# Optimization experiments

Measured on AMD Instinct MI355X. Metric: run time of the kernel, lower is better.

The kernel has to match this reference:

```python
import jax, jax.numpy as jnp
import numpy as np

B, Q, C = 1024, 300, 80   # batch, queries, classes
K = 300                   # num_top_queries


def setup_inputs() -> dict:
    key = jax.random.key(0)
    k1, k2, k3 = jax.random.split(key, 3)
    pred_logits = jax.random.normal(k1, (B, Q, C), dtype=jnp.float32)
    # cxcywh boxes normalized to [0,1]
    pred_boxes = jax.random.uniform(k2, (B, Q, 4), dtype=jnp.float32)
    # original image sizes (w, h) in pixels
    orig_target_sizes = jax.random.uniform(k3, (B, 2), dtype=jnp.float32) * 1333.0 + 1.0
    return {"pred_logits": pred_logits, "pred_boxes": pred_boxes,
            "orig_target_sizes": orig_target_sizes}


def reference(pred_logits, pred_boxes, orig_target_sizes):
    # box_convert cxcywh -> xyxy
    cx, cy, w, h = jnp.split(pred_boxes, 4, axis=-1)
    xyxy = jnp.concatenate([cx - 0.5 * w, cy - 0.5 * h,
                            cx + 0.5 * w, cy + 0.5 * h], axis=-1)  # [B,Q,4]
    # scale by (w,h,w,h) per image
    scale = jnp.tile(orig_target_sizes, (1, 2))[:, None, :]          # [B,1,4]
    bbox_pred = xyxy * scale                                         # [B,Q,4]

    # focal-loss branch: sigmoid + flattened topk
    scores_flat = jax.nn.sigmoid(pred_logits).reshape(B, Q * C)      # [B,Q*C]
    top_scores, index = jax.lax.top_k(scores_flat, K)                # [B,K]
    labels = index % C                                               # class id
    qidx = index // C                                                # query id
    boxes = jnp.take_along_axis(bbox_pred, qidx[..., None], axis=1)  # [B,K,4]
    return labels, boxes, top_scores
```

## Files before the change

kernel.cpp:

```cpp
#include <hip/hip_runtime.h>
#include <stdint.h>

#define NBATCH 1024
#define NQ 300
#define NC 80
#define QC 24000
#define NF4 6000
#define TOPK 300
#define RSEL 384u
#define NT 256
#define LG (NT / 64)
#define NV 24
#define TAIL 112
#define NB1 2048
#define SH1 21
#define SH2 13
#define SELCAP 2048
#define FINCAP 768
#define THRESH 2.0f
#define NBH 2048
#define RG (NBH / NT)
#define SBASE 0x3F600000u

__device__ __forceinline__ uint32_t xform(uint32_t u) {
    return u ^ (uint32_t)(((int32_t)u >> 31) | 0x80000000);
}

__device__ __forceinline__ uint32_t sbucket(uint32_t sbits) {
    int32_t d = (int32_t)(sbits - SBASE);
    d = d < 0 ? 0 : d;
    uint32_t bkt = ((uint32_t)d) >> 10;
    return bkt > (NBH - 1) ? (NBH - 1) : bkt;
}

template<int NB, bool ZERO>
__device__ __forceinline__ void pick(uint32_t* __restrict__ hist,
                                     uint32_t* __restrict__ part,
                                     uint32_t* __restrict__ gsufx,
                                     uint32_t* __restrict__ misc,
                                     int tid, uint32_t rem,
                                     uint32_t* bucket_out, uint32_t* rem_out) {
    constexpr int G = (NB >= NT) ? (NB / NT) : 1;
    const int base = tid * G;
    uint32_t h[G];
    uint32_t s = 0;
    if (base < NB) {
#pragma unroll
        for (int u = 0; u < G; ++u) { h[u] = hist[base + u]; s += h[u]; }
        if (ZERO) {
#pragma unroll
            for (int u = 0; u < G; ++u) hist[base + u] = 0;
        }
    } else {
#pragma unroll
        for (int u = 0; u < G; ++u) h[u] = 0;
    }
    part[tid] = s;
    __syncthreads();

    if (tid < 64) {
        uint32_t gs = 0;
#pragma unroll
        for (int u = 0; u < LG; ++u) gs += part[tid * LG + u];
        uint32_t S = gs;
#pragma unroll
        for (int off = 1; off < 64; off <<= 1) {
            uint32_t v = __shfl_down(S, off, 64);
            if (tid + off < 64) S += v;
        }
        gsufx[tid] = S;
        if (tid == 0) gsufx[64] = 0;
    }
    __syncthreads();

    const int g = tid / LG;
    uint32_t A = gsufx[g + 1];
    for (int t2 = tid + 1; t2 < (g + 1) * LG; ++t2) A += part[t2];
    if (base < NB && A < rem && A + s >= rem) {
        uint32_t acc = 0, bsel = (uint32_t)base, r = 1;
#pragma unroll
        for (int u = G - 1; u >= 0; --u) {
            if (A + acc + h[u] >= rem) { bsel = (uint32_t)(base + u); r = rem - A - acc; break; }
            acc += h[u];
        }
        misc[0] = bsel;
        misc[1] = r;
    }
    __syncthreads();
    *bucket_out = misc[0];
    *rem_out    = misc[1];
}

__global__ void __launch_bounds__(NT, 4)
rtdetr_post_kernel(const float* __restrict__ logits, const float* __restrict__ pboxes,
                   const float* __restrict__ sizes, float* __restrict__ out) {
    __shared__ __align__(16) uint32_t hist[NBH + 1];
    __shared__ uint64_t sel[SELCAP];
    __shared__ uint64_t sel2[FINCAP];
    __shared__ uint32_t part[NT];
    __shared__ uint32_t gsufx[65];
    __shared__ uint32_t misc[4];

    const int tid = threadIdx.x;
    const int b   = blockIdx.x;
    const float4* lg4 = reinterpret_cast<const float4*>(logits + (size_t)b * QC);

    for (int i = tid; i <= NBH; i += NT) hist[i] = 0;
    if (tid == 0) { misc[2] = 0; misc[3] = 0; }
    __syncthreads();

#pragma unroll
    for (int k = 0; k < NV; ++k) {
        if (k < NV - 1 || tid < TAIL) {
            const int i4 = tid + (k << 8);
            float4 v = lg4[i4];
            float f[4] = { v.x, v.y, v.z, v.w };
#pragma unroll
            for (int c = 0; c < 4; ++c) {
                if (f[c] >= THRESH) {
                    uint32_t key = xform(__float_as_uint(f[c]));
                    uint32_t pos = atomicAdd(&misc[2], 1u);
                    uint32_t idx = 4u * (uint32_t)i4 + (uint32_t)c;
                    if (pos < SELCAP)
                        sel[pos] = ((uint64_t)key << 32) | (uint64_t)(0xFFFFFFFFu - idx);
                }
            }
        }
    }
    __syncthreads();

    const uint32_t cnt = misc[2];
    uint32_t n2;

    if (cnt >= RSEL && cnt <= FINCAP) {
        for (uint32_t i = tid; i < cnt; i += NT) {
            uint64_t e = sel[i];
            uint32_t k = (uint32_t)(e >> 32);
            uint32_t bits = (k & 0x80000000u) ? (k & 0x7FFFFFFFu) : ~k;
            float x  = __uint_as_float(bits);
            float sc = 1.0f / (1.0f + expf(-x));
            sel2[i] = ((uint64_t)__float_as_uint(sc) << 32) | (uint64_t)(uint32_t)e;
        }
        n2 = cnt;
    } else {
        if (tid == 0) misc[2] = 0;
        __syncthreads();
        for (int i4 = tid; i4 < NF4; i4 += NT) {
            float4 v = lg4[i4];
            atomicAdd(&hist[xform(__float_as_uint(v.x)) >> SH1], 1u);
            atomicAdd(&hist[xform(__float_as_uint(v.y)) >> SH1], 1u);
            atomicAdd(&hist[xform(__float_as_uint(v.z)) >> SH1], 1u);
            atomicAdd(&hist[xform(__float_as_uint(v.w)) >> SH1], 1u);
        }
        __syncthreads();
        uint32_t b1, r1;
        pick<NB1, true>(hist, part, gsufx, misc, tid, RSEL, &b1, &r1);
        for (int i4 = tid; i4 < NF4; i4 += NT) {
            float4 v = lg4[i4];
            uint32_t kk[4] = { xform(__float_as_uint(v.x)), xform(__float_as_uint(v.y)),
                               xform(__float_as_uint(v.z)), xform(__float_as_uint(v.w)) };
#pragma unroll
            for (int c = 0; c < 4; ++c) {
                uint32_t k = kk[c];
                uint32_t bk = k >> SH1;
                if (bk >= b1) {
                    uint32_t pos = atomicAdd(&misc[2], 1u);
                    uint32_t idx = 4u * (uint32_t)i4 + (uint32_t)c;
                    if (pos < SELCAP)
                        sel[pos] = ((uint64_t)k << 32) | (uint64_t)(0xFFFFFFFFu - idx);
                    if (bk == b1) atomicAdd(&hist[(k >> SH2) & 0xFFu], 1u);
                }
            }
        }
        __syncthreads();
        uint32_t t2, r2;
        pick<256, false>(hist, part, gsufx, misc, tid, r1, &t2, &r2);
        (void)r2;
        const uint32_t T2 = (b1 << SH1) | (t2 << SH2);
        uint32_t c2 = misc[2];
        uint32_t nn = c2 > SELCAP ? SELCAP : c2;
        for (uint32_t i = tid; i < nn; i += NT) {
            uint64_t e = sel[i];
            uint32_t k = (uint32_t)(e >> 32);
            if (k >= T2) {
                uint32_t bits = (k & 0x80000000u) ? (k & 0x7FFFFFFFu) : ~k;
                float x  = __uint_as_float(bits);
                float sc = 1.0f / (1.0f + expf(-x));
                uint32_t pos = atomicAdd(&misc[3], 1u);
                if (pos < FINCAP)
                    sel2[pos] = ((uint64_t)__float_as_uint(sc) << 32) | (uint64_t)(uint32_t)e;
            }
        }
        __syncthreads();
        uint32_t m3 = misc[3];
        n2 = m3 > FINCAP ? FINCAP : m3;
        for (int i = tid; i < 256; i += NT) hist[i] = 0;
    }
    __syncthreads();

    for (uint32_t i = tid; i < n2; i += NT)
        atomicAdd(&hist[sbucket((uint32_t)(sel2[i] >> 32))], 1u);
    __syncthreads();

    {
        const int base = tid * RG;
        uint32_t h[RG];
        uint32_t s = 0;
#pragma unroll
        for (int u = 0; u < RG; ++u) { h[u] = hist[base + u]; s += h[u]; }
        part[tid] = s;
        __syncthreads();
        if (tid < 64) {
            uint32_t gs = 0;
#pragma unroll
            for (int u = 0; u < LG; ++u) gs += part[tid * LG + u];
            uint32_t S = gs;
#pragma unroll
            for (int off = 1; off < 64; off <<= 1) {
                uint32_t v = __shfl_down(S, off, 64);
                if (tid + off < 64) S += v;
            }
            gsufx[tid] = S;
            if (tid == 0) gsufx[64] = 0;
        }
        __syncthreads();
        const int g = tid / LG;
        uint32_t A = gsufx[g + 1];
        for (int t2 = tid + 1; t2 < (g + 1) * LG; ++t2) A += part[t2];
        uint32_t acc = A;
#pragma unroll
        for (int u = RG - 1; u >= 0; --u) { hist[base + u] = acc; acc += h[u]; }
    }
    __syncthreads();

    for (uint32_t i = tid; i < n2; i += NT) {
        uint64_t k = sel2[i];
        uint32_t slot = atomicAdd(&hist[sbucket((uint32_t)(k >> 32))], 1u);
        sel[slot] = k;
    }
    __syncthreads();

    for (uint32_t i = tid; i < n2; i += NT) {
        uint64_t my = sel2[i];
        uint32_t bkt = sbucket((uint32_t)(my >> 32));
        uint32_t seg0 = hist[bkt + 1];
        uint32_t seg1 = hist[bkt];
        uint32_t rank = seg0;
        for (uint32_t j = seg0; j < seg1; ++j)
            rank += (sel[j] > my) ? 1u : 0u;
        if (rank < TOPK) {
            uint32_t idx = 0xFFFFFFFFu - (uint32_t)(my & 0xFFFFFFFFull);
            uint32_t lab = idx % NC;
            uint32_t q   = idx / NC;
            float4 bx = reinterpret_cast<const float4*>(pboxes)[(size_t)b * NQ + q];
            float sw = sizes[2 * b + 0];
            float sh = sizes[2 * b + 1];
            float hw = 0.5f * bx.z, hh = 0.5f * bx.w;
            float4 o;
            o.x = (bx.x - hw) * sw;
            o.y = (bx.y - hh) * sh;
            o.z = (bx.x + hw) * sw;
            o.w = (bx.y + hh) * sh;
            out[(size_t)b * TOPK + rank] = (float)lab;
            reinterpret_cast<float4*>(out + (size_t)NBATCH * TOPK)[(size_t)b * TOPK + rank] = o;
            out[(size_t)NBATCH * TOPK * 5 + (size_t)b * TOPK + rank] =
                __uint_as_float((uint32_t)(my >> 32));
        }
    }
}

extern "C" void kernel_launch(void* const* d_in, const int* in_sizes, int n_in,
                              void* d_out, int out_size, void* d_ws, size_t ws_size,
                              hipStream_t stream) {
    const float* logits = (const float*)d_in[0];
    const float* pboxes = (const float*)d_in[1];
    const float* sizes  = (const float*)d_in[2];
    float* out = (float*)d_out;

    hipLaunchKernelGGL(rtdetr_post_kernel, dim3(NBATCH), dim3(NT), 0, stream,
                       logits, pboxes, sizes, out);
}
```

Before: 28.75 us.

## Split logits threshold scan into a multi-block streaming kernel plus a per-batch select kernel

The single per-batch kernel is split in two. The first kernel gives each batch row's logits to four blocks, which threshold-filter candidates into a global workspace with per-slice counts. The second kernel gathers those candidates into shared memory and runs the radix-select and rank. It also handles candidate counts up to SELCAP on the in-LDS path by taking histograms over the candidates instead of re-reading the logits, with a full rescan kept as the fallback. The aim is to spread the bandwidth-bound scan across four times as many blocks, at the cost of an extra launch and a workspace round trip.

```diff
diff --git a/kernel.cpp b/kernel.cpp
--- a/kernel.cpp
+++ b/kernel.cpp
@@ -8,10 +8,14 @@
 #define NF4 6000
 #define TOPK 300
 #define RSEL 384u
+#define NSLICE 4
+#define SELEM 6000
+#define SF4 1500
+#define NT1 256
+#define SEGCAP 768
 #define NT 256
 #define LG (NT / 64)
-#define NV 24
-#define TAIL 112
+#define RG (2048 / NT)
 #define NB1 2048
 #define SH1 21
 #define SH2 13
@@ -19,7 +23,6 @@
 #define FINCAP 768
 #define THRESH 2.0f
 #define NBH 2048
-#define RG (NBH / NT)
 #define SBASE 0x3F600000u
 
 __device__ __forceinline__ uint32_t xform(uint32_t u) {
@@ -31,6 +34,46 @@
     d = d < 0 ? 0 : d;
     uint32_t bkt = ((uint32_t)d) >> 10;
     return bkt > (NBH - 1) ? (NBH - 1) : bkt;
+}
+
+__global__ void __launch_bounds__(NT1, 8)
+k1_stream(const float* __restrict__ logits, uint32_t* __restrict__ cnts,
+          uint64_t* __restrict__ buf) {
+    __shared__ uint32_t scnt;
+    __shared__ uint64_t sbuf[SEGCAP];
+    const int tid = threadIdx.x;
+    const int blk = blockIdx.x;
+    const int b   = blk >> 2;
+    const int sl  = blk & 3;
+    const float4* lg4 = reinterpret_cast<const float4*>(logits + (size_t)b * QC) + sl * SF4;
+
+    if (tid == 0) scnt = 0;
+    __syncthreads();
+
+#pragma unroll
+    for (int k = 0; k < 6; ++k) {
+        const int i4 = tid + (k << 8);
+        if (k < 5 || i4 < SF4) {
+            float4 v = lg4[i4];
+            float f[4] = { v.x, v.y, v.z, v.w };
+#pragma unroll
+            for (int c = 0; c < 4; ++c) {
+                if (f[c] >= THRESH) {
+                    uint32_t key = xform(__float_as_uint(f[c]));
+                    uint32_t idx = (uint32_t)(sl * SELEM) + 4u * (uint32_t)i4 + (uint32_t)c;
+                    uint32_t pos = atomicAdd(&scnt, 1u);
+                    if (pos < SEGCAP)
+                        sbuf[pos] = ((uint64_t)key << 32) | (uint64_t)(0xFFFFFFFFu - idx);
+                }
+            }
+        }
+    }
+    __syncthreads();
+    const uint32_t n = scnt;
+    if (tid == 0) cnts[blk] = n;
+    const uint32_t m = n > SEGCAP ? SEGCAP : n;
+    for (uint32_t i = tid; i < m; i += NT1)
+        buf[(size_t)blk * SEGCAP + i] = sbuf[i];
 }
 
 template<int NB, bool ZERO>
@@ -92,59 +135,100 @@
 }
 
 __global__ void __launch_bounds__(NT, 4)
-rtdetr_post_kernel(const float* __restrict__ logits, const float* __restrict__ pboxes,
-                   const float* __restrict__ sizes, float* __restrict__ out) {
+k2_select(const float* __restrict__ logits, const float* __restrict__ pboxes,
+          const float* __restrict__ sizes, const uint32_t* __restrict__ cnts,
+          const uint64_t* __restrict__ buf, float* __restrict__ out) {
     __shared__ __align__(16) uint32_t hist[NBH + 1];
-    __shared__ uint64_t sel[SELCAP];
-    __shared__ uint64_t sel2[FINCAP];
+    __shared__ uint64_t cand[SELCAP];
+    __shared__ uint64_t srt[FINCAP];
     __shared__ uint32_t part[NT];
     __shared__ uint32_t gsufx[65];
     __shared__ uint32_t misc[4];
+    __shared__ uint32_t soff[NSLICE];
+    __shared__ uint32_t sinfo[2];
 
     const int tid = threadIdx.x;
     const int b   = blockIdx.x;
     const float4* lg4 = reinterpret_cast<const float4*>(logits + (size_t)b * QC);
 
     for (int i = tid; i <= NBH; i += NT) hist[i] = 0;
-    if (tid == 0) { misc[2] = 0; misc[3] = 0; }
-    __syncthreads();
-
-#pragma unroll
-    for (int k = 0; k < NV; ++k) {
-        if (k < NV - 1 || tid < TAIL) {
-            const int i4 = tid + (k << 8);
-            float4 v = lg4[i4];
-            float f[4] = { v.x, v.y, v.z, v.w };
-#pragma unroll
-            for (int c = 0; c < 4; ++c) {
-                if (f[c] >= THRESH) {
-                    uint32_t key = xform(__float_as_uint(f[c]));
-                    uint32_t pos = atomicAdd(&misc[2], 1u);
-                    uint32_t idx = 4u * (uint32_t)i4 + (uint32_t)c;
-                    if (pos < SELCAP)
-                        sel[pos] = ((uint64_t)key << 32) | (uint64_t)(0xFFFFFFFFu - idx);
-                }
-            }
-        }
-    }
-    __syncthreads();
-
-    const uint32_t cnt = misc[2];
+    if (tid == 0) {
+        uint32_t tot = 0, trunc = 0;
+        for (int s = 0; s < NSLICE; ++s) {
+            uint32_t c = cnts[b * NSLICE + s];
+            soff[s] = tot;
+            tot += c;
+            if (c > SEGCAP) trunc = 1;
+        }
+        sinfo[0] = tot; sinfo[1] = trunc;
+        misc[2] = 0; misc[3] = 0;
+    }
+    __syncthreads();
+
+    const uint32_t cnt   = sinfo[0];
+    const uint32_t trunc = sinfo[1];
+    const bool ldsResident = (!trunc && cnt <= SELCAP && cnt >= RSEL);
+
+    if (!trunc && cnt <= SELCAP) {
+#pragma unroll
+        for (int s = 0; s < NSLICE; ++s) {
+            uint32_t c = cnts[b * NSLICE + s];
+            uint32_t o = soff[s];
+            const uint64_t* src = buf + (size_t)(b * NSLICE + s) * SEGCAP;
+            for (uint32_t i = tid; i < c; i += NT) cand[o + i] = src[i];
+        }
+    }
+    __syncthreads();
+
     uint32_t n2;
 
-    if (cnt >= RSEL && cnt <= FINCAP) {
+    if (ldsResident && cnt <= FINCAP) {
         for (uint32_t i = tid; i < cnt; i += NT) {
-            uint64_t e = sel[i];
+            uint64_t e = cand[i];
             uint32_t k = (uint32_t)(e >> 32);
             uint32_t bits = (k & 0x80000000u) ? (k & 0x7FFFFFFFu) : ~k;
             float x  = __uint_as_float(bits);
             float sc = 1.0f / (1.0f + expf(-x));
-            sel2[i] = ((uint64_t)__float_as_uint(sc) << 32) | (uint64_t)(uint32_t)e;
+            uint32_t sb = __float_as_uint(sc);
+            srt[i] = ((uint64_t)sb << 32) | (uint64_t)(uint32_t)e;
+            atomicAdd(&hist[sbucket(sb)], 1u);
         }
         n2 = cnt;
+    } else if (ldsResident) {
+        for (uint32_t i = tid; i < cnt; i += NT)
+            atomicAdd(&hist[(uint32_t)(cand[i] >> 32) >> SH1], 1u);
+        __syncthreads();
+        uint32_t b1, r1;
+        pick<NB1, true>(hist, part, gsufx, misc, tid, RSEL, &b1, &r1);
+        for (uint32_t i = tid; i < cnt; i += NT) {
+            uint32_t k = (uint32_t)(cand[i] >> 32);
+            if ((k >> SH1) == b1) atomicAdd(&hist[(k >> SH2) & 0xFFu], 1u);
+        }
+        __syncthreads();
+        uint32_t t2, r2;
+        pick<256, false>(hist, part, gsufx, misc, tid, r1, &t2, &r2);
+        (void)r2;
+        const uint32_t T2 = (b1 << SH1) | (t2 << SH2);
+        for (uint32_t i = tid; i < cnt; i += NT) {
+            uint64_t e = cand[i];
+            uint32_t k = (uint32_t)(e >> 32);
+            if (k >= T2) {
+                uint32_t bits = (k & 0x80000000u) ? (k & 0x7FFFFFFFu) : ~k;
+                float x  = __uint_as_float(bits);
+                float sc = 1.0f / (1.0f + expf(-x));
+                uint32_t pos = atomicAdd(&misc[3], 1u);
+                if (pos < FINCAP)
+                    srt[pos] = ((uint64_t)__float_as_uint(sc) << 32) | (uint64_t)(uint32_t)e;
+            }
+        }
+        __syncthreads();
+        uint32_t m3 = misc[3];
+        n2 = m3 > FINCAP ? FINCAP : m3;
+        for (int i = tid; i < 256; i += NT) hist[i] = 0;
+        __syncthreads();
+        for (uint32_t i = tid; i < n2; i += NT)
+            atomicAdd(&hist[sbucket((uint32_t)(srt[i] >> 32))], 1u);
     } else {
-        if (tid == 0) misc[2] = 0;
-        __syncthreads();
         for (int i4 = tid; i4 < NF4; i4 += NT) {
             float4 v = lg4[i4];
             atomicAdd(&hist[xform(__float_as_uint(v.x)) >> SH1], 1u);
@@ -167,7 +251,7 @@
                     uint32_t pos = atomicAdd(&misc[2], 1u);
                     uint32_t idx = 4u * (uint32_t)i4 + (uint32_t)c;
                     if (pos < SELCAP)
-                        sel[pos] = ((uint64_t)k << 32) | (uint64_t)(0xFFFFFFFFu - idx);
+                        cand[pos] = ((uint64_t)k << 32) | (uint64_t)(0xFFFFFFFFu - idx);
                     if (bk == b1) atomicAdd(&hist[(k >> SH2) & 0xFFu], 1u);
                 }
             }
@@ -180,7 +264,7 @@
         uint32_t c2 = misc[2];
         uint32_t nn = c2 > SELCAP ? SELCAP : c2;
         for (uint32_t i = tid; i < nn; i += NT) {
-            uint64_t e = sel[i];
+            uint64_t e = cand[i];
             uint32_t k = (uint32_t)(e >> 32);
             if (k >= T2) {
                 uint32_t bits = (k & 0x80000000u) ? (k & 0x7FFFFFFFu) : ~k;
@@ -188,18 +272,17 @@
                 float sc = 1.0f / (1.0f + expf(-x));
                 uint32_t pos = atomicAdd(&misc[3], 1u);
                 if (pos < FINCAP)
-                    sel2[pos] = ((uint64_t)__float_as_uint(sc) << 32) | (uint64_t)(uint32_t)e;
+                    srt[pos] = ((uint64_t)__float_as_uint(sc) << 32) | (uint64_t)(uint32_t)e;
             }
         }
         __syncthreads();
         uint32_t m3 = misc[3];
         n2 = m3 > FINCAP ? FINCAP : m3;
         for (int i = tid; i < 256; i += NT) hist[i] = 0;
-    }
-    __syncthreads();
-
-    for (uint32_t i = tid; i < n2; i += NT)
-        atomicAdd(&hist[sbucket((uint32_t)(sel2[i] >> 32))], 1u);
+        __syncthreads();
+        for (uint32_t i = tid; i < n2; i += NT)
+            atomicAdd(&hist[sbucket((uint32_t)(srt[i] >> 32))], 1u);
+    }
     __syncthreads();
 
     {
@@ -234,20 +317,20 @@
     __syncthreads();
 
     for (uint32_t i = tid; i < n2; i += NT) {
-        uint64_t k = sel2[i];
+        uint64_t k = srt[i];
         uint32_t slot = atomicAdd(&hist[sbucket((uint32_t)(k >> 32))], 1u);
-        sel[slot] = k;
+        cand[slot] = k;
     }
     __syncthreads();
 
     for (uint32_t i = tid; i < n2; i += NT) {
-        uint64_t my = sel2[i];
+        uint64_t my = srt[i];
         uint32_t bkt = sbucket((uint32_t)(my >> 32));
         uint32_t seg0 = hist[bkt + 1];
         uint32_t seg1 = hist[bkt];
         uint32_t rank = seg0;
         for (uint32_t j = seg0; j < seg1; ++j)
-            rank += (sel[j] > my) ? 1u : 0u;
+            rank += (cand[j] > my) ? 1u : 0u;
         if (rank < TOPK) {
             uint32_t idx = 0xFFFFFFFFu - (uint32_t)(my & 0xFFFFFFFFull);
             uint32_t lab = idx % NC;
@@ -277,6 +360,11 @@
     const float* sizes  = (const float*)d_in[2];
     float* out = (float*)d_out;
 
-    hipLaunchKernelGGL(rtdetr_post_kernel, dim3(NBATCH), dim3(NT), 0, stream,
-                       logits, pboxes, sizes, out);
-}
+    uint32_t* cnts = (uint32_t*)d_ws;
+    uint64_t* buf  = (uint64_t*)((char*)d_ws + 16384);
+
+    hipLaunchKernelGGL(k1_stream, dim3(NBATCH * NSLICE), dim3(NT1), 0, stream,
+                       logits, cnts, buf);
+    hipLaunchKernelGGL(k2_select, dim3(NBATCH), dim3(NT), 0, stream,
+                       logits, pboxes, sizes, cnts, buf, out);
+}
```

Result: slower. 30.86 us (+7.3%).
